# Kernel tuning notes

Measured on AMD Instinct MI355X. Metric: run time of the kernel, lower is better.

## Reference

```python
import jax, jax.numpy as jnp
import numpy as np

N_NODES = 100000


def _gcn_conv(x, W, b, src, dst, norm, n):
    # PyG GCNConv: h = x @ W; out[i] = sum_j norm_ij * h[j]; out += b
    h = x @ W                                   # [N, F_out]
    msg = h[src] * norm[:, None]                # [E_total, F_out] gathered messages
    out = jax.ops.segment_sum(msg, dst, num_segments=n)
    return out + b


def _build_norm(edge_index, n):
    # add self loops, then symmetric normalization deg^-1/2 A_hat deg^-1/2
    loops = jnp.arange(n, dtype=edge_index.dtype)
    src = jnp.concatenate([edge_index[0], loops])
    dst = jnp.concatenate([edge_index[1], loops])
    deg = jnp.zeros((n,), jnp.float32).at[dst].add(1.0)
    dinv = jnp.where(deg > 0, jax.lax.rsqrt(deg), 0.0)
    norm = dinv[src] * dinv[dst]
    return src, dst, norm


def setup_inputs() -> dict:
    key = jax.random.key(0)
    k1, k2, k3 = jax.random.split(key, 3)
    d_in, d_hid, d_out = 128, 128, 64
    x = jax.random.normal(k1, (N_NODES, d_in), jnp.float32)
    edge_index = jax.random.randint(k2, (2, 1600000), 0, N_NODES, jnp.int64)
    kw1, kw2 = jax.random.split(k3)
    W1 = jax.random.normal(kw1, (d_in, d_hid), jnp.float32) * (1.0 / np.sqrt(d_in))
    b1 = jnp.zeros((d_hid,), jnp.float32)
    W2 = jax.random.normal(kw2, (d_hid, d_out), jnp.float32) * (1.0 / np.sqrt(d_hid))
    b2 = jnp.zeros((d_out,), jnp.float32)
    return {"x": x, "edge_index": edge_index, "W1": W1, "b1": b1, "W2": W2, "b2": b2}


def reference(x, edge_index, W1, b1, W2, b2):
    n = x.shape[0]
    src, dst, norm = _build_norm(edge_index, n)
    h = _gcn_conv(x, W1, b1, src, dst, norm, n)
    h = jax.nn.relu(h)
    # F.dropout(training=False) in eval mode is identity
    out = _gcn_conv(h, W2, b2, src, dst, norm, n)
    return out
```

## Files before the change

### kernel.cpp

```cpp
#include <hip/hip_runtime.h>
#include <hip/hip_fp16.h>

typedef _Float16 half8 __attribute__((ext_vector_type(8)));
typedef float f32x4 __attribute__((ext_vector_type(4)));

#define BUCKET_CAP 32768
#define BNODES 1024
#define NBSHIFT 10


__device__ __forceinline__ unsigned pack_half2(float x, float y) {
    __half2 h = __float22half2_rn(make_float2(x, y));
    return *reinterpret_cast<unsigned*>(&h);
}
__device__ __forceinline__ float2 up2(unsigned u) {
    __half2 h = *reinterpret_cast<__half2*>(&u);
    return __half22float2(h);
}
__device__ __forceinline__ void acc8(float4& a, uint2 v) {
    float2 p = up2(v.x), q = up2(v.y);
    a.x += p.x; a.y += p.y; a.z += q.x; a.w += q.y;
}
__device__ __forceinline__ void acc4(float2& a, unsigned v) {
    float2 p = up2(v);
    a.x += p.x; a.y += p.y;
}
__device__ __forceinline__ uint2 ld8(const char* __restrict__ b, unsigned off) {
    return *reinterpret_cast<const uint2*>(b + off);
}
__device__ __forceinline__ unsigned ld4(const char* __restrict__ b, unsigned off) {
    return *reinterpret_cast<const unsigned*>(b + off);
}


__global__ __launch_bounds__(256) void k_wconv(const float* __restrict__ W1,
                                               const float* __restrict__ W2,
                                               __half* __restrict__ Wt1,
                                               __half* __restrict__ Wt2,
                                               int* __restrict__ bcnt, int nbz) {
    int i = blockIdx.x * 256 + threadIdx.x;
    if (i < nbz) bcnt[i] = 0;
    if (i < 16384) {
        int col = i >> 7, k = i & 127;
        Wt1[i] = __float2half(W1[(k << 7) + col]);
    } else if (i < 24576) {
        int j = i - 16384;
        int col = j >> 7, k = j & 127;
        Wt2[j] = __float2half(W2[(k << 6) + col]);
    }
}


__global__ __launch_bounds__(256) void k_bscatter2(const int* __restrict__ src,
                                                   const int* __restrict__ dst, int E,
                                                   int* __restrict__ bcnt,
                                                   unsigned* __restrict__ pairs,
                                                   int NB, int epb) {
    __shared__ int h[128];
    __shared__ int base[128];
    for (int i = threadIdx.x; i < NB; i += 256) h[i] = 0;
    __syncthreads();
    int lo = blockIdx.x * epb;
    int hi = min(lo + epb, E);
    for (int e = lo + threadIdx.x; e < hi; e += 256)
        atomicAdd(&h[dst[e] >> NBSHIFT], 1);
    __syncthreads();
    for (int i = threadIdx.x; i < NB; i += 256) {
        int c = h[i];
        base[i] = c ? atomicAdd(&bcnt[i], c) : 0;
        h[i] = 0;
    }
    __syncthreads();
    for (int e = lo + threadIdx.x; e < hi; e += 256) {
        int s = src[e], d = dst[e];
        int b = d >> NBSHIFT;
        int r = atomicAdd(&h[b], 1);
        pairs[(size_t)b * BUCKET_CAP + base[b] + r] =
            (unsigned)s | ((unsigned)(d & (BNODES - 1)) << 17);
    }
}

__global__ __launch_bounds__(256) void k_bfinal2(const unsigned* __restrict__ pairs,
                                                 const int* __restrict__ bcnt,
                                                 float* __restrict__ dinv,
                                                 int* __restrict__ offs,
                                                 int* __restrict__ csc,
                                                 int n, int E, int NB) {
    __shared__ int cnt[BNODES];
    __shared__ int scn[256];
    __shared__ int cur[BNODES];
    int b = blockIdx.x, t = threadIdx.x;

    int part = 0;
    for (int i = t; i < b; i += 256) part += bcnt[i];
    scn[t] = part;
    __syncthreads();
    for (int d = 128; d > 0; d >>= 1) {
        if (t < d) scn[t] += scn[t + d];
        __syncthreads();
    }
    int cbase = scn[0];
    int cnt_b = bcnt[b];
    __syncthreads();

    for (int i = t; i < BNODES; i += 256) cnt[i] = 0;
    __syncthreads();
    size_t plo = (size_t)b * BUCKET_CAP;
    for (int e = t; e < cnt_b; e += 256)
        atomicAdd(&cnt[pairs[plo + e] >> 17], 1);
    __syncthreads();

    int c0 = cnt[4 * t], c1 = cnt[4 * t + 1], c2 = cnt[4 * t + 2], c3 = cnt[4 * t + 3];
    int tot = c0 + c1 + c2 + c3;
    __syncthreads();
    scn[t] = tot;
    __syncthreads();
    for (int d = 1; d < 256; d <<= 1) {
        int xv = (t >= d) ? scn[t - d] : 0;
        __syncthreads();
        scn[t] += xv;
        __syncthreads();
    }
    int basee = cbase + scn[t] - tot;
    int o0 = basee, o1 = basee + c0, o2 = o1 + c1, o3 = o2 + c2;
    int node0 = b * BNODES + 4 * t;
    if (node0 + 3 < n) {
        *reinterpret_cast<int4*>(offs + node0) = make_int4(o0, o1, o2, o3);
        *reinterpret_cast<float4*>(dinv + node0) =
            make_float4(rsqrtf((float)(c0 + 1)), rsqrtf((float)(c1 + 1)),
                        rsqrtf((float)(c2 + 1)), rsqrtf((float)(c3 + 1)));
    } else {
        if (node0 < n)     { offs[node0]     = o0; dinv[node0]     = rsqrtf((float)(c0 + 1)); }
        if (node0 + 1 < n) { offs[node0 + 1] = o1; dinv[node0 + 1] = rsqrtf((float)(c1 + 1)); }
        if (node0 + 2 < n) { offs[node0 + 2] = o2; dinv[node0 + 2] = rsqrtf((float)(c2 + 1)); }
    }
    if (b == NB - 1 && t == 255) offs[n] = E;
    cur[4 * t] = o0; cur[4 * t + 1] = o1; cur[4 * t + 2] = o2; cur[4 * t + 3] = o3;
    __syncthreads();
    for (int e = t; e < cnt_b; e += 256) {
        unsigned p = pairs[plo + e];
        int pos = atomicAdd(&cur[p >> 17], 1);
        csc[pos] = (int)(p & 0x1FFFFu);
    }
}


__global__ __launch_bounds__(256) void gemm1_mfma(const float* __restrict__ X,
                                                  const __half* __restrict__ Wt,
                                                  const float* __restrict__ dinv,
                                                  __half* __restrict__ H, int nrows) {
    __shared__ half8 wt[2048];
    const int t = threadIdx.x;

    const half8* Wg = reinterpret_cast<const half8*>(Wt);
    for (int i = t; i < 2048; i += 256) {
        int col = i >> 4, kc = i & 15;
        wt[(col << 4) | (kc ^ (col & 7))] = Wg[i];
    }

    const int wid = t >> 6, lane = t & 63;
    const int li = lane & 15, kq = lane >> 4;
    const int rbase = blockIdx.x * 64 + wid * 16;
    int row = rbase + li;
    int rowc = min(row, nrows - 1);

    const f32x4* X4 = reinterpret_cast<const f32x4*>(X) + (size_t)rowc * 32;
    half8 a[4];
#pragma unroll
    for (int kk = 0; kk < 4; ++kk) {
        f32x4 lo = __builtin_nontemporal_load(&X4[kk * 8 + kq * 2]);
        f32x4 hi = __builtin_nontemporal_load(&X4[kk * 8 + kq * 2 + 1]);
        half8 v;
        v[0] = (_Float16)lo[0]; v[1] = (_Float16)lo[1];
        v[2] = (_Float16)lo[2]; v[3] = (_Float16)lo[3];
        v[4] = (_Float16)hi[0]; v[5] = (_Float16)hi[1];
        v[6] = (_Float16)hi[2]; v[7] = (_Float16)hi[3];
        a[kk] = v;
    }
    __syncthreads();

    f32x4 acc[8];
#pragma unroll
    for (int ct = 0; ct < 8; ++ct) acc[ct] = (f32x4){0.f, 0.f, 0.f, 0.f};

#pragma unroll
    for (int ct = 0; ct < 8; ++ct) {
        int col = ct * 16 + li;
        int cbase = col << 4, sw = col & 7;
#pragma unroll
        for (int kk = 0; kk < 4; ++kk) {
            half8 b = wt[cbase | ((kk * 4 + kq) ^ sw)];
            acc[ct] = __builtin_amdgcn_mfma_f32_16x16x32_f16(a[kk], b, acc[ct], 0, 0, 0);
        }
    }

    const int r0 = rbase + kq * 4;
#pragma unroll
    for (int r = 0; r < 4; ++r) {
        int rr = r0 + r;
        if (rr < nrows) {
            float s = dinv[rr];
            __half* orow = H + (size_t)rr * 128;
#pragma unroll
            for (int ct = 0; ct < 8; ++ct)
                orow[ct * 16 + li] = __float2half(acc[ct][r] * s);
        }
    }
}

__global__ __launch_bounds__(256) void gemm2_mfma(const __half* __restrict__ Xh,
                                                  const __half* __restrict__ Wt,
                                                  const float* __restrict__ dinv,
                                                  __half* __restrict__ H, int nrows) {
    __shared__ half8 wt[1024];
    const int t = threadIdx.x;

    const half8* Wg = reinterpret_cast<const half8*>(Wt);
    for (int i = t; i < 1024; i += 256) {
        int col = i >> 4, kc = i & 15;
        wt[(col << 4) | (kc ^ (col & 7))] = Wg[i];
    }

    const int wid = t >> 6, lane = t & 63;
    const int li = lane & 15, kq = lane >> 4;
    const int rbase = blockIdx.x * 64 + wid * 16;
    int row = rbase + li;
    int rowc = min(row, nrows - 1);

    const half8* A8 = reinterpret_cast<const half8*>(Xh) + (size_t)rowc * 16;
    half8 a[4];
#pragma unroll
    for (int kk = 0; kk < 4; ++kk) a[kk] = A8[kk * 4 + kq];
    __syncthreads();

    f32x4 acc[4];
#pragma unroll
    for (int ct = 0; ct < 4; ++ct) acc[ct] = (f32x4){0.f, 0.f, 0.f, 0.f};

#pragma unroll
    for (int ct = 0; ct < 4; ++ct) {
        int col = ct * 16 + li;
        int cbase = col << 4, sw = col & 7;
#pragma unroll
        for (int kk = 0; kk < 4; ++kk) {
            half8 b = wt[cbase | ((kk * 4 + kq) ^ sw)];
            acc[ct] = __builtin_amdgcn_mfma_f32_16x16x32_f16(a[kk], b, acc[ct], 0, 0, 0);
        }
    }

    const int r0 = rbase + kq * 4;
#pragma unroll
    for (int r = 0; r < 4; ++r) {
        int rr = r0 + r;
        if (rr < nrows) {
            float s = dinv[rr];
            __half* orow = H + (size_t)rr * 64;
#pragma unroll
            for (int ct = 0; ct < 4; ++ct)
                orow[ct * 16 + li] = __float2half(acc[ct][r] * s);
        }
    }
}


__global__ __launch_bounds__(256) void k_agg1(const __half* __restrict__ h,
                                              const int* __restrict__ offs,
                                              const int* __restrict__ csc,
                                              const float* __restrict__ dinv,
                                              const float* __restrict__ bias,
                                              __half* __restrict__ out, int n) {
    int node = (blockIdx.x * 256 + threadIdx.x) >> 6;
    if (node >= n) return;
    int lane = threadIdx.x & 63;
    int g = lane >> 5, li = lane & 31;
    const char* hb = reinterpret_cast<const char*>(h);
    const unsigned loff = (unsigned)li << 3;
    int start = __builtin_amdgcn_readfirstlane(offs[node]);
    int end   = __builtin_amdgcn_readfirstlane(offs[node + 1]);
    float4 acc = make_float4(0.f, 0.f, 0.f, 0.f);

    int e = start;
    int emain = start + ((end - start) & ~7);
    for (; e < emain; e += 8) {
        int a0 = csc[e],     a1 = csc[e + 1], a2 = csc[e + 2], a3 = csc[e + 3];
        int a4 = csc[e + 4], a5 = csc[e + 5], a6 = csc[e + 6], a7 = csc[e + 7];
        unsigned o0 = (((unsigned)(g ? a1 : a0)) << 8) | loff;
        unsigned o1 = (((unsigned)(g ? a3 : a2)) << 8) | loff;
        unsigned o2 = (((unsigned)(g ? a5 : a4)) << 8) | loff;
        unsigned o3 = (((unsigned)(g ? a7 : a6)) << 8) | loff;
        uint2 v0 = ld8(hb, o0);
        uint2 v1 = ld8(hb, o1);
        uint2 v2 = ld8(hb, o2);
        uint2 v3 = ld8(hb, o3);
        acc8(acc, v0); acc8(acc, v1); acc8(acc, v2); acc8(acc, v3);
    }
    for (; e < end; e += 2) {
        int sa = csc[e];
        int sb = (e + 1 < end) ? csc[e + 1] : sa;
        unsigned o = (((unsigned)(g ? sb : sa)) << 8) | loff;
        uint2 v = ld8(hb, o);
        if (g && (e + 1 >= end)) { v.x = 0u; v.y = 0u; }
        acc8(acc, v);
    }
    acc.x += __shfl_xor(acc.x, 32);
    acc.y += __shfl_xor(acc.y, 32);
    acc.z += __shfl_xor(acc.z, 32);
    acc.w += __shfl_xor(acc.w, 32);
    uint2 vs = ld8(hb, (((unsigned)node) << 8) | loff);
    acc8(acc, vs);
    float di = dinv[node];
    float4 bb = reinterpret_cast<const float4*>(bias)[li];
    float ox = fmaxf(fmaf(acc.x, di, bb.x), 0.f);
    float oy = fmaxf(fmaf(acc.y, di, bb.y), 0.f);
    float oz = fmaxf(fmaf(acc.z, di, bb.z), 0.f);
    float ow = fmaxf(fmaf(acc.w, di, bb.w), 0.f);
    if (g == 0)
        reinterpret_cast<uint2*>(out)[(size_t)node * 32 + li] =
            make_uint2(pack_half2(ox, oy), pack_half2(oz, ow));
}

__global__ __launch_bounds__(256) void k_agg2(const __half* __restrict__ h,
                                              const int* __restrict__ offs,
                                              const int* __restrict__ csc,
                                              const float* __restrict__ dinv,
                                              const float* __restrict__ bias,
                                              float* __restrict__ out, int n) {
    int node = (blockIdx.x * 256 + threadIdx.x) >> 6;
    if (node >= n) return;
    int lane = threadIdx.x & 63;
    int g = lane >> 5, li = lane & 31;
    const char* hb = reinterpret_cast<const char*>(h);
    const unsigned loff = (unsigned)li << 2;
    int start = __builtin_amdgcn_readfirstlane(offs[node]);
    int end   = __builtin_amdgcn_readfirstlane(offs[node + 1]);
    float2 acc = make_float2(0.f, 0.f);

    int e = start;
    int emain = start + ((end - start) & ~7);
    for (; e < emain; e += 8) {
        int a0 = csc[e],     a1 = csc[e + 1], a2 = csc[e + 2], a3 = csc[e + 3];
        int a4 = csc[e + 4], a5 = csc[e + 5], a6 = csc[e + 6], a7 = csc[e + 7];
        unsigned o0 = (((unsigned)(g ? a1 : a0)) << 7) | loff;
        unsigned o1 = (((unsigned)(g ? a3 : a2)) << 7) | loff;
        unsigned o2 = (((unsigned)(g ? a5 : a4)) << 7) | loff;
        unsigned o3 = (((unsigned)(g ? a7 : a6)) << 7) | loff;
        unsigned v0 = ld4(hb, o0);
        unsigned v1 = ld4(hb, o1);
        unsigned v2 = ld4(hb, o2);
        unsigned v3 = ld4(hb, o3);
        acc4(acc, v0); acc4(acc, v1); acc4(acc, v2); acc4(acc, v3);
    }
    for (; e < end; e += 2) {
        int sa = csc[e];
        int sb = (e + 1 < end) ? csc[e + 1] : sa;
        unsigned o = (((unsigned)(g ? sb : sa)) << 7) | loff;
        unsigned v = ld4(hb, o);
        if (g && (e + 1 >= end)) v = 0u;
        acc4(acc, v);
    }
    acc.x += __shfl_xor(acc.x, 32);
    acc.y += __shfl_xor(acc.y, 32);
    acc4(acc, ld4(hb, (((unsigned)node) << 7) | loff));
    float di = dinv[node];
    float2 bb = reinterpret_cast<const float2*>(bias)[li];
    if (g == 0)
        reinterpret_cast<float2*>(out)[(size_t)node * 32 + li] =
            make_float2(fmaf(acc.x, di, bb.x), fmaf(acc.y, di, bb.y));
}


extern "C" void kernel_launch(void* const* d_in, const int* in_sizes, int n_in,
                              void* d_out, int out_size, void* d_ws, size_t ws_size,
                              hipStream_t stream) {
    const float* x  = (const float*)d_in[0];
    const int*   ei = (const int*)d_in[1];
    const float* W1 = (const float*)d_in[2];
    const float* b1 = (const float*)d_in[3];
    const float* W2 = (const float*)d_in[4];
    const float* b2 = (const float*)d_in[5];
    float* out = (float*)d_out;

    const int n = in_sizes[0] / 128;
    const int E = in_sizes[1] / 2;
    const int* src = ei;
    const int* dst = ei + E;
    const int NB = (n + BNODES - 1) / BNODES;

    char* p = (char*)d_ws;
    auto carve = [&](size_t bytes) -> void* {
        void* r = (void*)p;
        p += (bytes + 255) & ~(size_t)255;
        return r;
    };
    float* dinv    = (float*)carve((size_t)n * 4);
    int*   offs    = (int*)carve((size_t)(n + 1) * 4);
    int*   bcnt    = (int*)carve((size_t)(NB + 1) * 4);
    __half* Wt1h   = (__half*)carve(16384 * 2);
    __half* Wt2h   = (__half*)carve(8192 * 2);
    int*   csc     = (int*)carve((size_t)E * 4);
    __half* h1     = (__half*)carve((size_t)n * 128 * 2);
    __half* out1   = (__half*)carve((size_t)n * 128 * 2);
    unsigned* pairs = (unsigned*)h1;
    __half* h2     = h1;

    const int gmm  = (n + 63) / 64;
    const int gagg = (n + 3) / 4;
    const int GB   = 512;
    const int epb  = (E + GB - 1) / GB;

    k_wconv<<<96, 256, 0, stream>>>(W1, W2, Wt1h, Wt2h, bcnt, NB + 1);

    k_bscatter2<<<GB, 256, 0, stream>>>(src, dst, E, bcnt, pairs, NB, epb);
    k_bfinal2<<<NB, 256, 0, stream>>>(pairs, bcnt, dinv, offs, csc, n, E, NB);

    gemm1_mfma<<<gmm, 256, 0, stream>>>(x, Wt1h, dinv, h1, n);
    k_agg1<<<gagg, 256, 0, stream>>>(h1, offs, csc, dinv, b1, out1, n);

    gemm2_mfma<<<gmm, 256, 0, stream>>>(out1, Wt2h, dinv, h2, n);
    k_agg2<<<gagg, 256, 0, stream>>>(h2, offs, csc, dinv, b2, out, n);
}
```

Baseline: 203.5 us.

## Use 256-node buckets for CSC build with nontemporal pair stores

Shrinks destination buckets from 1024 to 256 nodes, which raises the bucket count to about 391 and reduces per-bucket capacity. The pair encoding becomes 24-bit source plus 8-bit local destination. The finalize kernel now has one node per thread with fewer shared arrays, and the scatter uses 128 blocks and nontemporal stores. The aim is more parallelism and less shared memory in the finalize pass, traded against more global atomics per scatter block. It also risks bucket overflow if any 256-node bucket receives more than 8192 edges.

```diff
diff --git a/kernel.cpp b/kernel.cpp
--- a/kernel.cpp
+++ b/kernel.cpp
@@ -4,9 +4,7 @@
 typedef _Float16 half8 __attribute__((ext_vector_type(8)));
 typedef float f32x4 __attribute__((ext_vector_type(4)));
 
-#define BUCKET_CAP 32768
-#define BNODES 1024
-#define NBSHIFT 10
+#define BUCKET_CAP 8192
 
 
 __device__ __forceinline__ unsigned pack_half2(float x, float y) {
@@ -56,14 +54,14 @@
                                                    int* __restrict__ bcnt,
                                                    unsigned* __restrict__ pairs,
                                                    int NB, int epb) {
-    __shared__ int h[128];
-    __shared__ int base[128];
+    __shared__ int h[512];
+    __shared__ int base[512];
     for (int i = threadIdx.x; i < NB; i += 256) h[i] = 0;
     __syncthreads();
     int lo = blockIdx.x * epb;
     int hi = min(lo + epb, E);
     for (int e = lo + threadIdx.x; e < hi; e += 256)
-        atomicAdd(&h[dst[e] >> NBSHIFT], 1);
+        atomicAdd(&h[dst[e] >> 8], 1);
     __syncthreads();
     for (int i = threadIdx.x; i < NB; i += 256) {
         int c = h[i];
@@ -73,10 +71,11 @@
     __syncthreads();
     for (int e = lo + threadIdx.x; e < hi; e += 256) {
         int s = src[e], d = dst[e];
-        int b = d >> NBSHIFT;
+        int b = d >> 8;
         int r = atomicAdd(&h[b], 1);
-        pairs[(size_t)b * BUCKET_CAP + base[b] + r] =
-            (unsigned)s | ((unsigned)(d & (BNODES - 1)) << 17);
+        __builtin_nontemporal_store(
+            (unsigned)s | ((unsigned)(d & 255) << 24),
+            &pairs[(size_t)b * BUCKET_CAP + base[b] + r]);
     }
 }
 
@@ -86,9 +85,8 @@
                                                  int* __restrict__ offs,
                                                  int* __restrict__ csc,
                                                  int n, int E, int NB) {
-    __shared__ int cnt[BNODES];
+    __shared__ int cnt[256];
     __shared__ int scn[256];
-    __shared__ int cur[BNODES];
     int b = blockIdx.x, t = threadIdx.x;
 
     int part = 0;
@@ -103,17 +101,16 @@
     int cnt_b = bcnt[b];
     __syncthreads();
 
-    for (int i = t; i < BNODES; i += 256) cnt[i] = 0;
+    cnt[t] = 0;
     __syncthreads();
     size_t plo = (size_t)b * BUCKET_CAP;
     for (int e = t; e < cnt_b; e += 256)
-        atomicAdd(&cnt[pairs[plo + e] >> 17], 1);
-    __syncthreads();
-
-    int c0 = cnt[4 * t], c1 = cnt[4 * t + 1], c2 = cnt[4 * t + 2], c3 = cnt[4 * t + 3];
-    int tot = c0 + c1 + c2 + c3;
-    __syncthreads();
-    scn[t] = tot;
+        atomicAdd(&cnt[pairs[plo + e] >> 24], 1);
+    __syncthreads();
+    int c = cnt[t];
+    int node = b * 256 + t;
+    if (node < n) dinv[node] = rsqrtf((float)(c + 1));
+    scn[t] = c;
     __syncthreads();
     for (int d = 1; d < 256; d <<= 1) {
         int xv = (t >= d) ? scn[t - d] : 0;
@@ -121,26 +118,15 @@
         scn[t] += xv;
         __syncthreads();
     }
-    int basee = cbase + scn[t] - tot;
-    int o0 = basee, o1 = basee + c0, o2 = o1 + c1, o3 = o2 + c2;
-    int node0 = b * BNODES + 4 * t;
-    if (node0 + 3 < n) {
-        *reinterpret_cast<int4*>(offs + node0) = make_int4(o0, o1, o2, o3);
-        *reinterpret_cast<float4*>(dinv + node0) =
-            make_float4(rsqrtf((float)(c0 + 1)), rsqrtf((float)(c1 + 1)),
-                        rsqrtf((float)(c2 + 1)), rsqrtf((float)(c3 + 1)));
-    } else {
-        if (node0 < n)     { offs[node0]     = o0; dinv[node0]     = rsqrtf((float)(c0 + 1)); }
-        if (node0 + 1 < n) { offs[node0 + 1] = o1; dinv[node0 + 1] = rsqrtf((float)(c1 + 1)); }
-        if (node0 + 2 < n) { offs[node0 + 2] = o2; dinv[node0 + 2] = rsqrtf((float)(c2 + 1)); }
-    }
+    int myoff = cbase + scn[t] - c;
+    if (node < n) offs[node] = myoff;
     if (b == NB - 1 && t == 255) offs[n] = E;
-    cur[4 * t] = o0; cur[4 * t + 1] = o1; cur[4 * t + 2] = o2; cur[4 * t + 3] = o3;
+    cnt[t] = myoff;
     __syncthreads();
     for (int e = t; e < cnt_b; e += 256) {
         unsigned p = pairs[plo + e];
-        int pos = atomicAdd(&cur[p >> 17], 1);
-        csc[pos] = (int)(p & 0x1FFFFu);
+        int pos = atomicAdd(&cnt[p >> 24], 1);
+        csc[pos] = (int)(p & 0x00FFFFFFu);
     }
 }
 
@@ -384,7 +370,7 @@
     const int E = in_sizes[1] / 2;
     const int* src = ei;
     const int* dst = ei + E;
-    const int NB = (n + BNODES - 1) / BNODES;
+    const int NB = (n + 255) / 256;
 
     char* p = (char*)d_ws;
     auto carve = [&](size_t bytes) -> void* {
@@ -405,7 +391,7 @@
 
     const int gmm  = (n + 63) / 64;
     const int gagg = (n + 3) / 4;
-    const int GB   = 512;
+    const int GB   = 128;
     const int epb  = (E + GB - 1) / GB;
 
     k_wconv<<<96, 256, 0, stream>>>(W1, W2, Wt1h, Wt2h, bcnt, NB + 1);
```

Result: slower. 215.8 us (+6.0%).
